# Performance work log

Hardware: AMD Instinct MI355X
Metric: run time of the kernel (lower is better)

## Reference

```python
import jax, jax.numpy as jnp
import numpy as np

B, S, H, V, L = 8, 1024, 1024, 512, 6
NEG_INF = -10000000.0  # matches torch neg_inf constant


def setup_inputs() -> dict:
    key = jax.random.key(0)
    ks = jax.random.split(key, 13)
    s = 0.02
    return {
        "inputs": jax.random.randint(ks[0], (B, S), 0, V),
        "embedding": jax.random.normal(ks[1], (V, H), jnp.float32) * s,
        "Wq": jax.random.normal(ks[2], (L, H, H), jnp.float32) * s,
        "bq": jnp.zeros((L, H), jnp.float32),
        "Wk": jax.random.normal(ks[3], (L, H, H), jnp.float32) * s,
        "bk": jnp.zeros((L, H), jnp.float32),
        "Wv": jax.random.normal(ks[4], (L, H, H), jnp.float32) * s,
        "bv": jnp.zeros((L, H), jnp.float32),
        "Wm": jax.random.normal(ks[5], (L, H, H), jnp.float32) * s,
        "bm": jnp.zeros((L, H), jnp.float32),
        "Wout": jax.random.normal(ks[6], (H, V), jnp.float32) * s,
        "bout": jnp.zeros((V,), jnp.float32),
    }


def reference(inputs, embedding, Wq, bq, Wk, bk, Wv, bv, Wm, bm, Wout, bout):
    Hd = embedding.shape[1]
    seq = inputs.shape[1]
    scale = jax.lax.rsqrt(jnp.asarray(Hd, jnp.float32))
    idx = jnp.arange(seq)
    # mask[key, query]: additive NEG_INF where key > query (strict lower triangle)
    mask = jnp.where(idx[:, None] > idx[None, :], jnp.float32(NEG_INF), jnp.float32(0.0))
    x = embedding[inputs]  # [B, S, H]
    n_layers = Wq.shape[0]
    attns = []
    for l in range(n_layers):
        q = x @ Wq[l] + bq[l]
        k = x @ Wk[l] + bk[l]
        v = x @ Wv[l] + bv[l]
        # [B, key, query], softmax over key axis (dim=1), exactly as original
        logits = jnp.einsum('bkh,bqh->bkq', k, q) * scale + mask
        attn = jax.nn.softmax(logits, axis=1)
        ctx = jnp.einsum('bkq,bkh->bqh', attn, v)  # attn^T @ v
        residual = x + ctx
        x = residual + jax.nn.relu(ctx @ Wm[l] + bm[l])
        attns.append(attn)
    out = x @ Wout + bout  # [B, S, V]
    return out, jnp.stack(attns)  # attns: [L, B, S, S]
```

## Files before the change

### kernel.cpp

```cpp
#include <hip/hip_runtime.h>
#include <stdint.h>

typedef unsigned short u16;
typedef unsigned int u32;
typedef __bf16 bf16x8 __attribute__((ext_vector_type(8)));
typedef float floatx4 __attribute__((ext_vector_type(4)));

#define NEG_INF_F (-10000000.0f)

__device__ __forceinline__ float bf2f(u16 u) {
    union { u32 u; float f; } x; x.u = ((u32)u) << 16; return x.f;
}
__device__ __forceinline__ u16 f2bf(float f) {
    union { float f; u32 u; } x; x.f = f;
    u32 r = x.u + 0x7fffu + ((x.u >> 16) & 1u);
    return (u16)(r >> 16);
}

__device__ __forceinline__ void async_cp16(const void* g, void* l) {
    __builtin_amdgcn_global_load_lds(
        (const __attribute__((address_space(1))) void*)g,
        (__attribute__((address_space(3))) void*)l, 16, 0, 0);
}

enum { EPI_QKV = 0, EPI_LOGITS = 1, EPI_CTX = 2, EPI_MLP = 3, EPI_OUT = 4 };

template <int EPI>
__global__ __launch_bounds__(256) void gemm_bt(
    const u16* __restrict__ A, int lda, long long aBatch,
    const u16* __restrict__ B, int ldb, long long bBatch,
    void* __restrict__ Cv, int ldc, long long cBatch,
    int K,
    const float* __restrict__ bias,
    float* __restrict__ xbuf,
    const u16* __restrict__ ctxb,
    u16* __restrict__ xb,
    float scale)
{
    __shared__ __align__(16) u16 sA[128 * 64];
    __shared__ __align__(16) u16 sB[128 * 64];

    const int tid  = threadIdx.x;
    const int wave = tid >> 6;
    const int lane = tid & 63;
    const int bz   = blockIdx.z;

    const u16* Ab = A + (long long)bz * aBatch + (long long)(blockIdx.y * 128) * lda;
    const u16* Bb = B + (long long)bz * bBatch + (long long)(blockIdx.x * 128) * ldb;

    const int wm = wave >> 1, wn = wave & 1;
    const int quad = lane >> 4;

    const int srowoff = lane >> 3;
    const int gf      = (lane & 7) ^ ((lane >> 3) & 7);

    const int ra = 64 * wm + (lane & 15);
    const int rb = 64 * wn + (lane & 15);
    const int rx7 = lane & 7;

    floatx4 zero = {0.f, 0.f, 0.f, 0.f};
    floatx4 acc[4][4];
#pragma unroll
    for (int i = 0; i < 4; ++i)
#pragma unroll
        for (int j = 0; j < 4; ++j) acc[i][j] = zero;

    for (int k0 = 0; k0 < K; k0 += 64) {
#pragma unroll
        for (int i = 0; i < 4; ++i) {
            const int c = wave * 4 + i;
            const int r = c * 8 + srowoff;
            async_cp16(Ab + (long long)r * lda + k0 + gf * 8, &sA[c * 512 + lane * 8]);
            async_cp16(Bb + (long long)r * ldb + k0 + gf * 8, &sB[c * 512 + lane * 8]);
        }
        __syncthreads();

#pragma unroll
        for (int kk = 0; kk < 64; kk += 32) {
            const int gbase = kk >> 3;
            const int ga = ((gbase + quad) ^ rx7) << 3;
            bf16x8 af[4], bf[4];
#pragma unroll
            for (int mi = 0; mi < 4; ++mi)
                af[mi] = *(const bf16x8*)&sA[(ra + 16 * mi) * 64 + ga];
#pragma unroll
            for (int ni = 0; ni < 4; ++ni)
                bf[ni] = *(const bf16x8*)&sB[(rb + 16 * ni) * 64 + ga];
#pragma unroll
            for (int mi = 0; mi < 4; ++mi)
#pragma unroll
                for (int ni = 0; ni < 4; ++ni)
                    acc[mi][ni] = __builtin_amdgcn_mfma_f32_16x16x32_bf16(
                        af[mi], bf[ni], acc[mi][ni], 0, 0, 0);
        }
        __syncthreads();
    }

    const int m0 = blockIdx.y * 128 + 64 * wm + (quad << 2);
    const int n0 = blockIdx.x * 128 + 64 * wn + (lane & 15);
#pragma unroll
    for (int mi = 0; mi < 4; ++mi) {
#pragma unroll
        for (int ni = 0; ni < 4; ++ni) {
            const int gn = n0 + ni * 16;
#pragma unroll
            for (int r = 0; r < 4; ++r) {
                const int gm = m0 + mi * 16 + r;
                float v = acc[mi][ni][r];
                if constexpr (EPI == EPI_QKV) {
                    v += bias[gn];
                    ((u16*)Cv)[(long long)bz * cBatch + (long long)gm * ldc + gn] = f2bf(v);
                } else if constexpr (EPI == EPI_LOGITS) {
                    v = v * scale + (gm > gn ? NEG_INF_F : 0.0f);
                    ((float*)Cv)[(long long)bz * cBatch + (long long)gm * ldc + gn] = v;
                } else if constexpr (EPI == EPI_CTX) {
                    ((u16*)Cv)[(long long)bz * cBatch + (long long)gm * ldc + gn] = f2bf(v);
                } else if constexpr (EPI == EPI_MLP) {
                    const long long idx = (long long)gm * ldc + gn;
                    v += bias[gn];
                    v = fmaxf(v, 0.0f);
                    float xv = xbuf[idx] + bf2f(ctxb[idx]) + v;
                    xbuf[idx] = xv;
                    xb[idx]   = f2bf(xv);
                } else {
                    v += bias[gn];
                    ((float*)Cv)[(long long)gm * ldc + gn] = v;
                }
            }
        }
    }
}

template <typename Tin>
__global__ void transpose_bf16(const Tin* __restrict__ in, int inStride, long long inBatch,
                               u16* __restrict__ out, int outStride, long long outBatch)
{
    __shared__ float tile[64][65];
    const Tin* ib = in + (long long)blockIdx.z * inBatch;
    u16* ob       = out + (long long)blockIdx.z * outBatch;
    const int r0 = blockIdx.y * 64, c0 = blockIdx.x * 64;
    const int x = threadIdx.x, y = threadIdx.y;
#pragma unroll
    for (int j = 0; j < 16; ++j) {
        int r = y + j * 4;
        float v;
        if constexpr (sizeof(Tin) == 2)
            v = bf2f(((const u16*)ib)[(long long)(r0 + r) * inStride + c0 + x]);
        else
            v = ((const float*)ib)[(long long)(r0 + r) * inStride + c0 + x];
        tile[r][x] = v;
    }
    __syncthreads();
#pragma unroll
    for (int j = 0; j < 16; ++j) {
        int r = y + j * 4;
        ob[(long long)(c0 + r) * outStride + r0 + x] = f2bf(tile[x][r]);
    }
}

__global__ __launch_bounds__(1024) void softmax_emit(
    float* __restrict__ attn, long long batchStride,
    u16* __restrict__ attnT, long long tBatchStride)
{
    __shared__ float sm[64][16], sl[64][16], sm2[8][16], sl2[8][16];
    __shared__ float sM[16], sInv[16];

    float* base = attn + (long long)blockIdx.y * batchStride;
    const int x = threadIdx.x, ky = threadIdx.y;
    const int q = blockIdx.x * 16 + x;

    float v[16];
    float m = -3.4e38f, l = 0.f;
#pragma unroll
    for (int j = 0; j < 16; ++j) {
        v[j] = base[(long long)(ky * 16 + j) * 1024 + q];
        float mn = fmaxf(m, v[j]);
        l = l * __expf(m - mn) + __expf(v[j] - mn);
        m = mn;
    }
    sm[ky][x] = m;
    sl[ky][x] = l;
    __syncthreads();
    if (ky < 8) {
        float M = -3.4e38f, L = 0.f;
#pragma unroll
        for (int t = 0; t < 8; ++t) {
            float mm = sm[ky + 8 * t][x], ll = sl[ky + 8 * t][x];
            float mn = fmaxf(M, mm);
            L = L * __expf(M - mn) + ll * __expf(mm - mn);
            M = mn;
        }
        sm2[ky][x] = M;
        sl2[ky][x] = L;
    }
    __syncthreads();
    if (ky == 0) {
        float M = -3.4e38f, L = 0.f;
#pragma unroll
        for (int t = 0; t < 8; ++t) {
            float mm = sm2[t][x], ll = sl2[t][x];
            float mn = fmaxf(M, mm);
            L = L * __expf(M - mn) + ll * __expf(mm - mn);
            M = mn;
        }
        sM[x]   = M;
        sInv[x] = 1.0f / L;
    }
    __syncthreads();
    const float M = sM[x], inv = sInv[x];

    u16 pb[16];
#pragma unroll
    for (int j = 0; j < 16; ++j) {
        float p = __expf(v[j] - M) * inv;
        base[(long long)(ky * 16 + j) * 1024 + q] = p;
        pb[j] = f2bf(p);
    }
    u16* trow = attnT + (long long)blockIdx.y * tBatchStride + (long long)q * 1024 + ky * 16;
    ((uint4*)trow)[0] = *(const uint4*)&pb[0];
    ((uint4*)trow)[1] = *(const uint4*)&pb[8];
}

__global__ void embed_kernel(const int* __restrict__ tok, const float* __restrict__ emb,
                             float* __restrict__ x, u16* __restrict__ xb)
{
    const int row = blockIdx.x;
    const int t   = tok[row];
    float4 v = ((const float4*)(emb + (long long)t * 1024))[threadIdx.x];
    ((float4*)(x + (long long)row * 1024))[threadIdx.x] = v;
    uint2 p;
    p.x = (u32)f2bf(v.x) | ((u32)f2bf(v.y) << 16);
    p.y = (u32)f2bf(v.z) | ((u32)f2bf(v.w) << 16);
    ((uint2*)(xb + (long long)row * 1024))[threadIdx.x] = p;
}

__global__ void pack_bias(const float* __restrict__ bq, const float* __restrict__ bk,
                          const float* __restrict__ bv, float* __restrict__ out)
{
    int i = blockIdx.x * 256 + threadIdx.x;
    int l = i / 3072, j = i % 3072;
    float v = (j < 1024) ? bq[l * 1024 + j]
            : (j < 2048) ? bk[l * 1024 + j - 1024]
                         : bv[l * 1024 + j - 2048];
    out[i] = v;
}

extern "C" void kernel_launch(void* const* d_in, const int* in_sizes, int n_in,
                              void* d_out, int out_size, void* d_ws, size_t ws_size,
                              hipStream_t stream)
{
    const int*   tok  = (const int*)d_in[0];
    const float* emb  = (const float*)d_in[1];
    const float* Wq   = (const float*)d_in[2];
    const float* bq   = (const float*)d_in[3];
    const float* Wk   = (const float*)d_in[4];
    const float* bk   = (const float*)d_in[5];
    const float* Wv   = (const float*)d_in[6];
    const float* bv   = (const float*)d_in[7];
    const float* Wm   = (const float*)d_in[8];
    const float* bm   = (const float*)d_in[9];
    const float* Wout = (const float*)d_in[10];
    const float* bout = (const float*)d_in[11];
    float* out = (float*)d_out;

    constexpr int B = 8, S = 1024, H = 1024, V = 512, L = 6;
    constexpr long long M = (long long)B * S;

    char* ws = (char*)d_ws;
    u16*   WqkvT = (u16*)ws;   ws += (long long)L * 3 * H * H * 2;
    u16*   WmT   = (u16*)ws;   ws += (long long)L * H * H * 2;
    u16*   WoutT = (u16*)ws;   ws += (long long)V * H * 2;
    float* bqkv  = (float*)ws; ws += (long long)L * 3 * H * 4;
    float* x     = (float*)ws; ws += M * H * 4;
    u16*   xb    = (u16*)ws;   ws += M * H * 2;
    u16*   QKV   = (u16*)ws;   ws += M * 3 * H * 2;
    u16*   attnT = (u16*)ws;   ws += (long long)B * S * S * 2;
    u16*   Vt    = (u16*)ws;   ws += (long long)B * S * S * 2;
    u16*   ctxb  = (u16*)ws;   ws += M * H * 2;

    float* attnOut = out + (long long)B * S * V;

    const dim3 tb(64, 4);
    transpose_bf16<float><<<dim3(16, 16, L), tb, 0, stream>>>(
        Wq, H, (long long)H * H, WqkvT, H, (long long)3 * H * H);
    transpose_bf16<float><<<dim3(16, 16, L), tb, 0, stream>>>(
        Wk, H, (long long)H * H, WqkvT + (long long)H * H, H, (long long)3 * H * H);
    transpose_bf16<float><<<dim3(16, 16, L), tb, 0, stream>>>(
        Wv, H, (long long)H * H, WqkvT + (long long)2 * H * H, H, (long long)3 * H * H);
    transpose_bf16<float><<<dim3(16, 16, L), tb, 0, stream>>>(
        Wm, H, (long long)H * H, WmT, H, (long long)H * H);
    transpose_bf16<float><<<dim3(V / 64, 16, 1), tb, 0, stream>>>(
        Wout, V, 0, WoutT, H, 0);
    pack_bias<<<(L * 3 * H) / 256, 256, 0, stream>>>(bq, bk, bv, bqkv);
    embed_kernel<<<M, 256, 0, stream>>>(tok, emb, x, xb);

    for (int l = 0; l < L; ++l) {
        gemm_bt<EPI_QKV><<<dim3(3 * H / 128, M / 128, 1), 256, 0, stream>>>(
            xb, H, 0, WqkvT + (long long)l * 3 * H * H, H, 0,
            QKV, 3 * H, 0, H, bqkv + l * 3 * H, nullptr, nullptr, nullptr, 0.f);

        float* attnL = attnOut + (long long)l * B * S * S;
        gemm_bt<EPI_LOGITS><<<dim3(S / 128, S / 128, B), 256, 0, stream>>>(
            QKV + H, 3 * H, (long long)S * 3 * H,
            QKV, 3 * H, (long long)S * 3 * H,
            attnL, S, (long long)S * S, H,
            nullptr, nullptr, nullptr, nullptr, 0.03125f);

        softmax_emit<<<dim3(S / 16, B), dim3(16, 64), 0, stream>>>(
            attnL, (long long)S * S, attnT, (long long)S * S);

        transpose_bf16<u16><<<dim3(16, 16, B), tb, 0, stream>>>(
            QKV + 2 * H, 3 * H, (long long)S * 3 * H, Vt, S, (long long)S * S);

        gemm_bt<EPI_CTX><<<dim3(H / 128, S / 128, B), 256, 0, stream>>>(
            attnT, S, (long long)S * S, Vt, S, (long long)S * S,
            ctxb, H, (long long)S * H, S,
            nullptr, nullptr, nullptr, nullptr, 0.f);

        gemm_bt<EPI_MLP><<<dim3(H / 128, M / 128, 1), 256, 0, stream>>>(
            ctxb, H, 0, WmT + (long long)l * H * H, H, 0,
            nullptr, H, 0, H, bm + l * H, x, ctxb, xb, 0.f);
    }

    gemm_bt<EPI_OUT><<<dim3(V / 128, M / 128, 1), 256, 0, stream>>>(
        xb, H, 0, WoutT, H, 0, out, V, 0, H,
        bout, nullptr, nullptr, nullptr, 0.f);
}
```

Before: 1.543 ms.

## Skip masked causal tiles in logits and context GEMMs; fuse weight setup

The logits GEMM now launches only the 36 upper-triangular 128x128 tiles per batch, mapping a linear block index to a (key, query) tile pair. The context GEMM truncates its K loop to the keys that can be nonzero for each query tile. Softmax no longer loads masked entries and substitutes the mask constant instead, so fully masked logits are never stored or read. The separate weight-transpose and bias-pack launches are merged into one setup kernel, which cuts launch overhead. The masked region of the attention output relies on softmax writing zeros there, and the tiles get uneven per-block work.

```diff
diff --git a/kernel.cpp b/kernel.cpp
--- a/kernel.cpp
+++ b/kernel.cpp
@@ -45,8 +45,20 @@
     const int lane = tid & 63;
     const int bz   = blockIdx.z;
 
-    const u16* Ab = A + (long long)bz * aBatch + (long long)(blockIdx.y * 128) * lda;
-    const u16* Bb = B + (long long)bz * bBatch + (long long)(blockIdx.x * 128) * ldb;
+    int bxE = blockIdx.x, byE = blockIdx.y;
+    if constexpr (EPI == EPI_LOGITS) {
+        const int t = blockIdx.x;
+        int tq = (int)((sqrtf(8.0f * t + 1.0f) - 1.0f) * 0.5f);
+        while ((tq + 1) * (tq + 2) / 2 <= t) ++tq;
+        while (tq * (tq + 1) / 2 > t) --tq;
+        bxE = tq;
+        byE = t - tq * (tq + 1) / 2;
+    }
+    int Keff = K;
+    if constexpr (EPI == EPI_CTX) Keff = min(K, (byE + 1) * 128);
+
+    const u16* Ab = A + (long long)bz * aBatch + (long long)(byE * 128) * lda;
+    const u16* Bb = B + (long long)bz * bBatch + (long long)(bxE * 128) * ldb;
 
     const int wm = wave >> 1, wn = wave & 1;
     const int quad = lane >> 4;
@@ -65,7 +77,7 @@
 #pragma unroll
         for (int j = 0; j < 4; ++j) acc[i][j] = zero;
 
-    for (int k0 = 0; k0 < K; k0 += 64) {
+    for (int k0 = 0; k0 < Keff; k0 += 64) {
 #pragma unroll
         for (int i = 0; i < 4; ++i) {
             const int c = wave * 4 + i;
@@ -96,8 +108,8 @@
         __syncthreads();
     }
 
-    const int m0 = blockIdx.y * 128 + 64 * wm + (quad << 2);
-    const int n0 = blockIdx.x * 128 + 64 * wn + (lane & 15);
+    const int m0 = byE * 128 + 64 * wm + (quad << 2);
+    const int n0 = bxE * 128 + 64 * wn + (lane & 15);
 #pragma unroll
     for (int mi = 0; mi < 4; ++mi) {
 #pragma unroll
@@ -158,6 +170,61 @@
     }
 }
 
+template <int L, int H, int V>
+__global__ void setup_weights(const float* __restrict__ Wq, const float* __restrict__ Wk,
+                              const float* __restrict__ Wv, const float* __restrict__ Wm,
+                              const float* __restrict__ Wout,
+                              const float* __restrict__ bq, const float* __restrict__ bk,
+                              const float* __restrict__ bv,
+                              u16* __restrict__ WqkvT, u16* __restrict__ WmT,
+                              u16* __restrict__ WoutT, float* __restrict__ bqkv)
+{
+    const int z = blockIdx.z;
+    if (z == 4 * L + 1) {
+        int i = ((blockIdx.y * 16 + blockIdx.x) * 256) + threadIdx.y * 64 + threadIdx.x;
+        if (i < L * 3 * H) {
+            int l = i / (3 * H), j = i % (3 * H);
+            float v = (j < H) ? bq[l * H + j]
+                    : (j < 2 * H) ? bk[l * H + j - H]
+                                  : bv[l * H + j - 2 * H];
+            bqkv[i] = v;
+        }
+        return;
+    }
+
+    const float* in;
+    u16* outp;
+    int inStride, outStride;
+    if (z == 4 * L) {
+        if (blockIdx.x >= V / 64) return;
+        in = Wout; inStride = V;
+        outp = WoutT; outStride = H;
+    } else {
+        const int which = z / L, l = z % L;
+        inStride = H; outStride = H;
+        if (which == 3) { in = Wm + (long long)l * H * H; outp = WmT + (long long)l * H * H; }
+        else {
+            in   = (which == 0 ? Wq : which == 1 ? Wk : Wv) + (long long)l * H * H;
+            outp = WqkvT + (long long)l * 3 * H * H + (long long)which * H * H;
+        }
+    }
+
+    __shared__ float tile[64][65];
+    const int r0 = blockIdx.y * 64, c0 = blockIdx.x * 64;
+    const int x = threadIdx.x, y = threadIdx.y;
+#pragma unroll
+    for (int j = 0; j < 16; ++j) {
+        int r = y + j * 4;
+        tile[r][x] = in[(long long)(r0 + r) * inStride + c0 + x];
+    }
+    __syncthreads();
+#pragma unroll
+    for (int j = 0; j < 16; ++j) {
+        int r = y + j * 4;
+        outp[(long long)(c0 + r) * outStride + r0 + x] = f2bf(tile[x][r]);
+    }
+}
+
 __global__ __launch_bounds__(1024) void softmax_emit(
     float* __restrict__ attn, long long batchStride,
     u16* __restrict__ attnT, long long tBatchStride)
@@ -173,9 +240,12 @@
     float m = -3.4e38f, l = 0.f;
 #pragma unroll
     for (int j = 0; j < 16; ++j) {
-        v[j] = base[(long long)(ky * 16 + j) * 1024 + q];
-        float mn = fmaxf(m, v[j]);
-        l = l * __expf(m - mn) + __expf(v[j] - mn);
+        const int k = ky * 16 + j;
+        float vj = NEG_INF_F;
+        if (k <= q) vj = base[(long long)k * 1024 + q];
+        v[j] = vj;
+        float mn = fmaxf(m, vj);
+        l = l * __expf(m - mn) + __expf(vj - mn);
         m = mn;
     }
     sm[ky][x] = m;
@@ -232,17 +302,6 @@
     p.x = (u32)f2bf(v.x) | ((u32)f2bf(v.y) << 16);
     p.y = (u32)f2bf(v.z) | ((u32)f2bf(v.w) << 16);
     ((uint2*)(xb + (long long)row * 1024))[threadIdx.x] = p;
-}
-
-__global__ void pack_bias(const float* __restrict__ bq, const float* __restrict__ bk,
-                          const float* __restrict__ bv, float* __restrict__ out)
-{
-    int i = blockIdx.x * 256 + threadIdx.x;
-    int l = i / 3072, j = i % 3072;
-    float v = (j < 1024) ? bq[l * 1024 + j]
-            : (j < 2048) ? bk[l * 1024 + j - 1024]
-                         : bv[l * 1024 + j - 2048];
-    out[i] = v;
 }
 
 extern "C" void kernel_launch(void* const* d_in, const int* in_sizes, int n_in,
@@ -280,18 +339,8 @@
 
     float* attnOut = out + (long long)B * S * V;
 
-    const dim3 tb(64, 4);
-    transpose_bf16<float><<<dim3(16, 16, L), tb, 0, stream>>>(
-        Wq, H, (long long)H * H, WqkvT, H, (long long)3 * H * H);
-    transpose_bf16<float><<<dim3(16, 16, L), tb, 0, stream>>>(
-        Wk, H, (long long)H * H, WqkvT + (long long)H * H, H, (long long)3 * H * H);
-    transpose_bf16<float><<<dim3(16, 16, L), tb, 0, stream>>>(
-        Wv, H, (long long)H * H, WqkvT + (long long)2 * H * H, H, (long long)3 * H * H);
-    transpose_bf16<float><<<dim3(16, 16, L), tb, 0, stream>>>(
-        Wm, H, (long long)H * H, WmT, H, (long long)H * H);
-    transpose_bf16<float><<<dim3(V / 64, 16, 1), tb, 0, stream>>>(
-        Wout, V, 0, WoutT, H, 0);
-    pack_bias<<<(L * 3 * H) / 256, 256, 0, stream>>>(bq, bk, bv, bqkv);
+    setup_weights<L, H, V><<<dim3(16, 16, 4 * L + 2), dim3(64, 4), 0, stream>>>(
+        Wq, Wk, Wv, Wm, Wout, bq, bk, bv, WqkvT, WmT, WoutT, bqkv);
     embed_kernel<<<M, 256, 0, stream>>>(tok, emb, x, xb);
 
     for (int l = 0; l < L; ++l) {
@@ -300,7 +349,7 @@
             QKV, 3 * H, 0, H, bqkv + l * 3 * H, nullptr, nullptr, nullptr, 0.f);
 
         float* attnL = attnOut + (long long)l * B * S * S;
-        gemm_bt<EPI_LOGITS><<<dim3(S / 128, S / 128, B), 256, 0, stream>>>(
+        gemm_bt<EPI_LOGITS><<<dim3(36, 1, B), 256, 0, stream>>>(
             QKV + H, 3 * H, (long long)S * 3 * H,
             QKV, 3 * H, (long long)S * 3 * H,
             attnL, S, (long long)S * S, H,
@@ -309,7 +358,7 @@
         softmax_emit<<<dim3(S / 16, B), dim3(16, 64), 0, stream>>>(
             attnL, (long long)S * S, attnT, (long long)S * S);
 
-        transpose_bf16<u16><<<dim3(16, 16, B), tb, 0, stream>>>(
+        transpose_bf16<u16><<<dim3(16, 16, B), dim3(64, 4), 0, stream>>>(
             QKV + 2 * H, 3 * H, (long long)S * 3 * H, Vt, S, (long long)S * S);
 
         gemm_bt<EPI_CTX><<<dim3(H / 128, S / 128, B), 256, 0, stream>>>(
```

Result: faster. 1.490 ms (-3.4%).
